# Kernel optimization log

Hardware: AMD Instinct MI355X
Metric: run time of the kernel (lower is better)

## Reference

```python
import jax, jax.numpy as jnp
import numpy as np

DIM_V = 512
NUM_HEADS = 8
LN_EPS = 1e-5


def _layernorm(x):
    # LayerNorm over last dim, no affine (simplified_layer_norm=True)
    mu = jnp.mean(x, axis=-1, keepdims=True)
    var = jnp.mean(jnp.square(x - mu), axis=-1, keepdims=True)
    return (x - mu) * jax.lax.rsqrt(var + LN_EPS)


def setup_inputs() -> dict:
    key = jax.random.key(0)
    ks = jax.random.split(key, 12)
    B, Nq, Nk, dQ, dK, dV = 16, 1024, 1024, 512, 512, DIM_V
    s = 0.02
    return {
        "Q": jax.random.normal(ks[0], (B, Nq, dQ), jnp.float32),
        "K": jax.random.normal(ks[1], (B, Nk, dK), jnp.float32),
        "Wq": jax.random.normal(ks[2], (dQ, dV), jnp.float32) * s,
        "bq": jnp.zeros((dV,), jnp.float32),
        "Wk": jax.random.normal(ks[3], (dK, dV), jnp.float32) * s,
        "bk": jnp.zeros((dV,), jnp.float32),
        "Wv": jax.random.normal(ks[4], (dK, dV), jnp.float32) * s,
        "bv": jnp.zeros((dV,), jnp.float32),
        "Wo": jax.random.normal(ks[5], (dV, dV), jnp.float32) * s,
        "bo": jnp.zeros((dV,), jnp.float32),
    }


def reference(Q, K, Wq, bq, Wk, bk, Wv, bv, Wo, bo):
    H = NUM_HEADS
    dh = DIM_V // H
    q = Q @ Wq + bq            # [B, Nq, dV]
    k = K @ Wk + bk            # [B, Nk, dV]
    v = K @ Wv + bv            # [B, Nk, dV]
    B, Nq, _ = q.shape
    Nk = k.shape[1]
    qh = q.reshape(B, Nq, H, dh)
    kh = k.reshape(B, Nk, H, dh)
    vh = v.reshape(B, Nk, H, dh)
    # NOTE: faithful to source — scale by sqrt(dim_V), not sqrt(head_dim)
    scores = jnp.einsum('bqhd,bkhd->bhqk', qh, kh) / jnp.sqrt(jnp.asarray(DIM_V, q.dtype))
    A = jax.nn.softmax(scores, axis=-1)                    # [B, H, Nq, Nk]
    attn = jnp.einsum('bhqk,bkhd->bqhd', A, vh).reshape(B, Nq, DIM_V)
    O = q + attn               # residual with projected Q
    O = _layernorm(O)          # ln0 (no affine)
    O = O + jax.nn.gelu(O @ Wo + bo, approximate=False)
    O = _layernorm(O)          # ln1 (no affine)
    return O
```

## Files before the change

kernel.cpp:

```cpp
#include <hip/hip_runtime.h>
#include <hip/hip_bf16.h>
#include <math.h>

typedef __bf16 bf16;
typedef __bf16 bf16x8 __attribute__((ext_vector_type(8)));
typedef float  f32x4  __attribute__((ext_vector_type(4)));

#define MFMA16(a,b,c) __builtin_amdgcn_mfma_f32_16x16x32_bf16((a),(b),(c),0,0,0)
#define ATT_SCALE_LOG2E 0.0637587160330163f

__device__ __forceinline__ void async16p(const void* g, void* l) {
    __builtin_amdgcn_global_load_lds((const __attribute__((address_space(1))) void*)g,
                                     (__attribute__((address_space(3))) void*)l,
                                     16, 0, 0);
}

__global__ __launch_bounds__(256) void prep_kernel(
    const float* __restrict__ Q, const float* __restrict__ K,
    const float* __restrict__ Wq, const float* __restrict__ Wk,
    const float* __restrict__ Wv, const float* __restrict__ Wo,
    bf16* __restrict__ Qb, bf16* __restrict__ Kb,
    bf16* __restrict__ WqT, bf16* __restrict__ WkT,
    bf16* __restrict__ WvT, bf16* __restrict__ WoT)
{
    __shared__ float tile[32][33];
    const int bx = blockIdx.x;
    if (bx < 8192) {
        const float* src = (bx < 4096) ? Q : K;
        bf16* dst        = (bx < 4096) ? Qb : Kb;
        int i = ((bx & 4095) * 256 + threadIdx.x) * 8;
        float4 a = *(const float4*)(src + i);
        float4 b = *(const float4*)(src + i + 4);
        bf16x8 o;
        o[0]=(bf16)a.x; o[1]=(bf16)a.y; o[2]=(bf16)a.z; o[3]=(bf16)a.w;
        o[4]=(bf16)b.x; o[5]=(bf16)b.y; o[6]=(bf16)b.z; o[7]=(bf16)b.w;
        *(bf16x8*)(dst + i) = o;
    } else {
        const int wid = bx - 8192;
        const float* W; bf16* T;
        switch (wid >> 8) {
          case 0: W=Wq; T=WqT; break;
          case 1: W=Wk; T=WkT; break;
          case 2: W=Wv; T=WvT; break;
          default: W=Wo; T=WoT; break;
        }
        const int rest = wid & 255;
        const int k0 = (rest & 15) * 32, n0 = (rest >> 4) * 32;
        const int tx = threadIdx.x & 31, ty = threadIdx.x >> 5;
        #pragma unroll
        for (int i=0;i<32;i+=8)
            tile[ty+i][tx] = W[(size_t)(k0+ty+i)*512 + n0+tx];
        __syncthreads();
        #pragma unroll
        for (int i=0;i<32;i+=8)
            T[(size_t)(n0+ty+i)*512 + k0+tx] = (bf16)tile[tx][ty+i];
    }
}

__device__ __forceinline__ void gemm_core(
    const bf16* __restrict__ A, const bf16* __restrict__ BT,
    int m0, int n0, char* smem, f32x4 (&acc)[4][4])
{
    bf16* As = (bf16*)smem;
    bf16* Bs = (bf16*)(smem + 16384);
    const int tid = threadIdx.x;
    const int lane = tid & 63, wave = tid >> 6;
    const int qd = lane >> 4, lr = lane & 15;
    const int wm = (wave & 1) * 64, wn = (wave >> 1) * 64;

    const int srow = tid >> 3;
    const int sgr  = ((tid & 7) ^ (srow & 7)) * 8;
    const bf16* gA = A  + (size_t)(m0 + srow)*512 + sgr;
    const bf16* gB = BT + (size_t)(n0 + srow)*512 + sgr;
    bf16* lA = As + wave*512;
    bf16* lB = Bs + wave*512;

    for (int k0 = 0; k0 < 512; k0 += 64) {
        __syncthreads();
        #pragma unroll
        for (int i=0;i<4;i++) {
            async16p(gA + k0 + (size_t)i*32*512, lA + i*2048);
            async16p(gB + k0 + (size_t)i*32*512, lB + i*2048);
        }
        __syncthreads();
        #pragma unroll
        for (int half=0; half<2; ++half) {
            bf16x8 af[4], bfr[4];
            #pragma unroll
            for (int mi=0;mi<4;mi++) {
                int row = wm + mi*16 + lr;
                af[mi] = *(bf16x8*)(As + row*64 + (((half*4+qd)^(lr&7))*8));
            }
            #pragma unroll
            for (int ni=0;ni<4;ni++) {
                int row = wn + ni*16 + lr;
                bfr[ni] = *(bf16x8*)(Bs + row*64 + (((half*4+qd)^(lr&7))*8));
            }
            #pragma unroll
            for (int mi=0;mi<4;mi++)
              #pragma unroll
              for (int ni=0;ni<4;ni++)
                acc[mi][ni] = MFMA16(af[mi], bfr[ni], acc[mi][ni]);
        }
    }
}

__global__ __launch_bounds__(256, 4) void gemm_qkv_kernel(
    const bf16* __restrict__ Qb, const bf16* __restrict__ Kb,
    const bf16* __restrict__ WqT, const bf16* __restrict__ WkT,
    const bf16* __restrict__ WvT,
    const float* __restrict__ bq, const float* __restrict__ bk,
    const float* __restrict__ bv,
    bf16* __restrict__ qbb, bf16* __restrict__ kbb, bf16* __restrict__ vT)
{
    __shared__ __align__(16) char smem[32768];
    const int z = blockIdx.z;
    const bf16* A  = (z == 0) ? Qb  : Kb;
    const bf16* BT = (z == 0) ? WqT : (z == 1) ? WkT : WvT;
    const float* bb = (z == 0) ? bq : (z == 1) ? bk  : bv;
    const int m0 = blockIdx.x * 128, n0 = blockIdx.y * 128;
    const int tid = threadIdx.x;
    const int lane = tid & 63, wave = tid >> 6;
    const int qd = lane >> 4, lr = lane & 15;
    const int wm = (wave & 1) * 64, wn = (wave >> 1) * 64;

    f32x4 acc[4][4];
    #pragma unroll
    for (int i=0;i<4;i++)
      #pragma unroll
      for (int j=0;j<4;j++) acc[i][j] = (f32x4){0,0,0,0};

    gemm_core(A, BT, m0, n0, smem, acc);

    if (z < 2) {
        bf16* C = (z == 0) ? qbb : kbb;
        #pragma unroll
        for (int ni=0;ni<4;ni++) {
            int n = n0 + wn + ni*16 + lr;
            float bv0 = bb[n];
            #pragma unroll
            for (int mi=0;mi<4;mi++) {
                int mb = m0 + wm + mi*16 + qd*4;
                #pragma unroll
                for (int r=0;r<4;r++)
                    C[(size_t)(mb+r)*512 + n] = (bf16)(acc[mi][ni][r] + bv0);
            }
        }
    } else {
        bf16* Lt = (bf16*)smem;
        const int b = m0 >> 10, tok0 = m0 & 1023;
        const int row = tid >> 2, ch = tid & 3;
        #pragma unroll
        for (int half = 0; half < 2; ++half) {
            __syncthreads();
            if ((wn >> 6) == half) {
                #pragma unroll
                for (int ni=0;ni<4;ni++) {
                    int nl = ni*16 + lr;
                    float bvv = bb[n0 + half*64 + nl];
                    #pragma unroll
                    for (int mi=0;mi<4;mi++)
                      #pragma unroll
                      for (int r=0;r<4;r++) {
                        int col = wm + mi*16 + qd*4 + r;
                        Lt[nl*128 + ((((col>>3)^(nl&7))<<3) | (col&7))]
                            = (bf16)(acc[mi][ni][r] + bvv);
                      }
                }
            }
            __syncthreads();
            const int h = (n0 >> 6) + half;
            bf16* dst = vT + ((size_t)((b*8 + h)*64 + row))*1024 + tok0 + ch*32;
            #pragma unroll
            for (int s=0;s<4;s++) {
                int g = (ch*4 + s) ^ (row & 7);
                *(uint4*)(dst + s*8) = *(uint4*)(Lt + row*128 + g*8);
            }
        }
    }
}

__global__ __launch_bounds__(256, 4) void attn_kernel(
    const bf16* __restrict__ qb, const bf16* __restrict__ kb,
    const bf16* __restrict__ vT, bf16* __restrict__ attnb)
{
    const int qt = blockIdx.x, h = blockIdx.y, b = blockIdx.z;
    const int tid = threadIdx.x, lane = tid & 63, wave = tid >> 6;
    const int qd = lane >> 4, lr = lane & 15;
    const int q0 = qt*128 + wave*32;

    __shared__ bf16 Ks[64*64];
    __shared__ bf16 Vs[64*64];
    __shared__ bf16 Pl[4][32][72];

    bf16x8 aq[2][2];
    #pragma unroll
    for (int mi=0;mi<2;mi++) {
        const bf16* qrow = qb + ((size_t)(b*1024 + q0 + mi*16 + lr))*512 + h*64;
        aq[mi][0] = *(const bf16x8*)(qrow + qd*8);
        aq[mi][1] = *(const bf16x8*)(qrow + 32 + qd*8);
    }

    const int srow = tid >> 2;
    const int c2 = (tid & 3) * 2;
    const int wg0 = ((c2  ) ^ (srow & 7)) * 8;
    const int wg1 = ((c2+1) ^ (srow & 7)) * 8;
    const bf16* kgp = kb + ((size_t)(b*1024 + srow))*512 + h*64 + c2*8;
    const bf16* vgp = vT + ((size_t)((b*8 + h)*64 + srow))*1024 + c2*8;

    uint4 k0r = *(const uint4*)(kgp);
    uint4 k1r = *(const uint4*)(kgp + 8);
    uint4 v0r = *(const uint4*)(vgp);
    uint4 v1r = *(const uint4*)(vgp + 8);

    f32x4 acc[2][4];
    #pragma unroll
    for (int mi=0;mi<2;mi++)
      #pragma unroll
      for (int ni=0;ni<4;ni++) acc[mi][ni] = (f32x4){0,0,0,0};
    float l[2][4] = {{0,0,0,0},{0,0,0,0}};

    for (int t=0; t<16; ++t) {
        __syncthreads();
        *(uint4*)(&Ks[srow*64 + wg0]) = k0r;
        *(uint4*)(&Ks[srow*64 + wg1]) = k1r;
        *(uint4*)(&Vs[srow*64 + wg0]) = v0r;
        *(uint4*)(&Vs[srow*64 + wg1]) = v1r;
        __syncthreads();
        if (t < 15) {
            const size_t kk = (size_t)(t+1)*64;
            k0r = *(const uint4*)(kgp + kk*512);
            k1r = *(const uint4*)(kgp + kk*512 + 8);
            v0r = *(const uint4*)(vgp + kk);
            v1r = *(const uint4*)(vgp + kk + 8);
        }

        f32x4 s[2][4];
        #pragma unroll
        for (int mi=0;mi<2;mi++)
          #pragma unroll
          for (int ni=0;ni<4;ni++) s[mi][ni] = (f32x4){0,0,0,0};
        #pragma unroll
        for (int ni=0;ni<4;ni++) {
            int row = ni*16 + lr;
            bf16x8 b0 = *(bf16x8*)(Ks + row*64 + (((qd  )^(lr&7))*8));
            bf16x8 b1 = *(bf16x8*)(Ks + row*64 + (((qd+4)^(lr&7))*8));
            #pragma unroll
            for (int mi=0;mi<2;mi++) {
                s[mi][ni] = MFMA16(aq[mi][0], b0, s[mi][ni]);
                s[mi][ni] = MFMA16(aq[mi][1], b1, s[mi][ni]);
            }
        }
        #pragma unroll
        for (int mi=0;mi<2;mi++)
          #pragma unroll
          for (int ni=0;ni<4;ni++)
            #pragma unroll
            for (int r=0;r<4;r++) {
                float pv = exp2f(s[mi][ni][r] * ATT_SCALE_LOG2E);
                s[mi][ni][r] = pv;
                l[mi][r] += pv;
            }
        #pragma unroll
        for (int mi=0;mi<2;mi++)
          #pragma unroll
          for (int ni=0;ni<4;ni++)
            #pragma unroll
            for (int r=0;r<4;r++)
                Pl[wave][mi*16 + qd*4 + r][ni*16 + lr] = (bf16)s[mi][ni][r];
        bf16x8 ap[2][2];
        #pragma unroll
        for (int mi=0;mi<2;mi++) {
            ap[mi][0] = *(bf16x8*)(&Pl[wave][mi*16+lr][qd*8]);
            ap[mi][1] = *(bf16x8*)(&Pl[wave][mi*16+lr][32+qd*8]);
        }
        #pragma unroll
        for (int ni=0;ni<4;ni++) {
            int row = ni*16 + lr;
            bf16x8 v0 = *(bf16x8*)(Vs + row*64 + (((qd  )^(lr&7))*8));
            bf16x8 v1 = *(bf16x8*)(Vs + row*64 + (((qd+4)^(lr&7))*8));
            #pragma unroll
            for (int mi=0;mi<2;mi++) {
                acc[mi][ni] = MFMA16(ap[mi][0], v0, acc[mi][ni]);
                acc[mi][ni] = MFMA16(ap[mi][1], v1, acc[mi][ni]);
            }
        }
    }

    #pragma unroll
    for (int off=1; off<16; off<<=1)
      #pragma unroll
      for (int mi=0;mi<2;mi++)
        #pragma unroll
        for (int r=0;r<4;r++) l[mi][r] += __shfl_xor(l[mi][r], off);

    #pragma unroll
    for (int mi=0;mi<2;mi++) {
        float inv[4];
        #pragma unroll
        for (int r=0;r<4;r++) inv[r] = 1.f / l[mi][r];
        #pragma unroll
        for (int ni=0;ni<4;ni++)
          #pragma unroll
          for (int r=0;r<4;r++)
            Pl[wave][qd*4+r][ni*16+lr] = (bf16)(acc[mi][ni][r] * inv[r]);
        bf16x8 oA = *(bf16x8*)(&Pl[wave][lr][qd*8]);
        bf16x8 oB = *(bf16x8*)(&Pl[wave][lr][32+qd*8]);
        bf16* dst = attnb + ((size_t)(b*1024 + q0 + mi*16 + lr))*512 + h*64;
        *(bf16x8*)(dst + qd*8)      = oA;
        *(bf16x8*)(dst + 32 + qd*8) = oB;
    }
}

__global__ __launch_bounds__(256) void ln0_kernel(
    const bf16* __restrict__ qbb, const bf16* __restrict__ attnb,
    bf16* __restrict__ Obf)
{
    const int wave = threadIdx.x >> 6, lane = threadIdx.x & 63;
    const int row = blockIdx.x*4 + wave;
    const size_t base = (size_t)row*512 + lane*8;
    bf16x8 qv = *(const bf16x8*)(qbb + base);
    bf16x8 av = *(const bf16x8*)(attnb + base);
    float x[8];
    #pragma unroll
    for (int i=0;i<8;i++) x[i] = (float)qv[i] + (float)av[i];
    float s1 = 0.f, s2 = 0.f;
    #pragma unroll
    for (int i=0;i<8;i++){ s1 += x[i]; s2 += x[i]*x[i]; }
    #pragma unroll
    for (int off=1; off<64; off<<=1) { s1 += __shfl_xor(s1, off); s2 += __shfl_xor(s2, off); }
    float mu  = s1 * (1.f/512.f);
    float var = s2 * (1.f/512.f) - mu*mu;
    float rstd = rsqrtf(var + 1e-5f);
    bf16x8 ob;
    #pragma unroll
    for (int i=0;i<8;i++) ob[i] = (bf16)((x[i]-mu)*rstd);
    *(bf16x8*)(Obf + base) = ob;
}

__global__ __launch_bounds__(256, 4) void gemm_o_kernel(
    const bf16* __restrict__ Obf, const bf16* __restrict__ WoT,
    const float* __restrict__ bo, bf16* __restrict__ xb)
{
    __shared__ __align__(16) char smem[32768];
    const int m0 = blockIdx.x * 128, n0 = blockIdx.y * 128;
    const int tid = threadIdx.x;
    const int lane = tid & 63, wave = tid >> 6;
    const int qd = lane >> 4, lr = lane & 15;
    const int wm = (wave & 1) * 64, wn = (wave >> 1) * 64;

    f32x4 acc[4][4];
    #pragma unroll
    for (int i=0;i<4;i++)
      #pragma unroll
      for (int j=0;j<4;j++) acc[i][j] = (f32x4){0,0,0,0};

    gemm_core(Obf, WoT, m0, n0, smem, acc);

    #pragma unroll
    for (int ni=0;ni<4;ni++) {
        int n = n0 + wn + ni*16 + lr;
        float bv = bo[n];
        #pragma unroll
        for (int mi=0;mi<4;mi++) {
            int mb = m0 + wm + mi*16 + qd*4;
            #pragma unroll
            for (int r=0;r<4;r++) {
                float g = acc[mi][ni][r] + bv;
                float gelu = 0.5f * g * (1.f + erff(g * 0.70710678118654752f));
                size_t idx = (size_t)(mb+r)*512 + n;
                xb[idx] = (bf16)((float)Obf[idx] + gelu);
            }
        }
    }
}

__global__ __launch_bounds__(256) void ln1_kernel(
    const bf16* __restrict__ xb, float* __restrict__ out)
{
    const int wave = threadIdx.x >> 6, lane = threadIdx.x & 63;
    const int row = blockIdx.x*4 + wave;
    const size_t base = (size_t)row*512 + lane*8;
    bf16x8 xv = *(const bf16x8*)(xb + base);
    float x[8];
    #pragma unroll
    for (int i=0;i<8;i++) x[i] = (float)xv[i];
    float s1 = 0.f, s2 = 0.f;
    #pragma unroll
    for (int i=0;i<8;i++){ s1 += x[i]; s2 += x[i]*x[i]; }
    #pragma unroll
    for (int off=1; off<64; off<<=1) { s1 += __shfl_xor(s1, off); s2 += __shfl_xor(s2, off); }
    float mu  = s1 * (1.f/512.f);
    float var = s2 * (1.f/512.f) - mu*mu;
    float rstd = rsqrtf(var + 1e-5f);
    float4 o0 = {(x[0]-mu)*rstd,(x[1]-mu)*rstd,(x[2]-mu)*rstd,(x[3]-mu)*rstd};
    float4 o1 = {(x[4]-mu)*rstd,(x[5]-mu)*rstd,(x[6]-mu)*rstd,(x[7]-mu)*rstd};
    *(float4*)(out + base)     = o0;
    *(float4*)(out + base + 4) = o1;
}

extern "C" void kernel_launch(void* const* d_in, const int* in_sizes, int n_in,
                              void* d_out, int out_size, void* d_ws, size_t ws_size,
                              hipStream_t stream)
{
    (void)in_sizes; (void)n_in; (void)out_size; (void)ws_size;
    const float* Q  = (const float*)d_in[0];
    const float* K  = (const float*)d_in[1];
    const float* Wq = (const float*)d_in[2];
    const float* bq = (const float*)d_in[3];
    const float* Wk = (const float*)d_in[4];
    const float* bk = (const float*)d_in[5];
    const float* Wv = (const float*)d_in[6];
    const float* bv = (const float*)d_in[7];
    const float* Wo = (const float*)d_in[8];
    const float* bo = (const float*)d_in[9];
    float* out = (float*)d_out;

    const size_t nTok = (size_t)16*1024*512;
    char* p = (char*)d_ws;
    auto alloc = [&](size_t bytes)->char* {
        char* r = p; p += (bytes + 255) & ~(size_t)255; return r;
    };
    bf16* Qb    = (bf16*)alloc(nTok*2);
    bf16* Kb    = (bf16*)alloc(nTok*2);
    bf16* WqT   = (bf16*)alloc(512*512*2);
    bf16* WkT   = (bf16*)alloc(512*512*2);
    bf16* WvT   = (bf16*)alloc(512*512*2);
    bf16* WoT   = (bf16*)alloc(512*512*2);
    bf16* qbb   = (bf16*)alloc(nTok*2);
    bf16* kbb   = (bf16*)alloc(nTok*2);
    bf16* vT    = (bf16*)alloc(nTok*2);
    bf16* attnb = (bf16*)alloc(nTok*2);
    bf16* Obf   = (bf16*)alloc(nTok*2);
    bf16* xb    = (bf16*)alloc(nTok*2);

    prep_kernel<<<9216, 256, 0, stream>>>(Q, K, Wq, Wk, Wv, Wo,
                                          Qb, Kb, WqT, WkT, WvT, WoT);
    gemm_qkv_kernel<<<dim3(128,4,3), 256, 0, stream>>>(Qb, Kb, WqT, WkT, WvT,
                                                       bq, bk, bv, qbb, kbb, vT);
    attn_kernel<<<dim3(8,8,16), 256, 0, stream>>>(qbb, kbb, vT, attnb);
    ln0_kernel<<<4096, 256, 0, stream>>>(qbb, attnb, Obf);
    gemm_o_kernel<<<dim3(128,4), 256, 0, stream>>>(Obf, WoT, bo, xb);
    ln1_kernel<<<4096, 256, 0, stream>>>(xb, out);
}
```

Before: 294.9 us.

## Fuse fp32-to-bf16 input conversion into QKV GEMM and residual into attention

Drops the separate pass that converts Q and K to bf16. The QKV GEMM now loads fp32 tiles straight into shared memory and converts them while building MFMA fragments, with the K-step halved to 32. The residual add of projected q is moved into the attention epilogue, so ln0 no longer reads qbb. The attention K/V shared tiles switch from an XOR swizzle to a padded layout, and exp2 with a folded log2e becomes __expf. This removes a full fp32 read/bf16 write round trip of the inputs, but the fp32 A tile doubles shared traffic per element and occupancy is lowered to 3.

```diff
diff --git a/kernel.cpp b/kernel.cpp
--- a/kernel.cpp
+++ b/kernel.cpp
@@ -7,7 +7,7 @@
 typedef float  f32x4  __attribute__((ext_vector_type(4)));
 
 #define MFMA16(a,b,c) __builtin_amdgcn_mfma_f32_16x16x32_bf16((a),(b),(c),0,0,0)
-#define ATT_SCALE_LOG2E 0.0637587160330163f
+#define ATT_SCALE 0.0441941738241592f
 
 __device__ __forceinline__ void async16p(const void* g, void* l) {
     __builtin_amdgcn_global_load_lds((const __attribute__((address_space(1))) void*)g,
@@ -15,122 +15,96 @@
                                      16, 0, 0);
 }
 
-__global__ __launch_bounds__(256) void prep_kernel(
-    const float* __restrict__ Q, const float* __restrict__ K,
+__global__ __launch_bounds__(256) void prep_w_kernel(
     const float* __restrict__ Wq, const float* __restrict__ Wk,
     const float* __restrict__ Wv, const float* __restrict__ Wo,
-    bf16* __restrict__ Qb, bf16* __restrict__ Kb,
     bf16* __restrict__ WqT, bf16* __restrict__ WkT,
     bf16* __restrict__ WvT, bf16* __restrict__ WoT)
 {
     __shared__ float tile[32][33];
     const int bx = blockIdx.x;
-    if (bx < 8192) {
-        const float* src = (bx < 4096) ? Q : K;
-        bf16* dst        = (bx < 4096) ? Qb : Kb;
-        int i = ((bx & 4095) * 256 + threadIdx.x) * 8;
-        float4 a = *(const float4*)(src + i);
-        float4 b = *(const float4*)(src + i + 4);
-        bf16x8 o;
-        o[0]=(bf16)a.x; o[1]=(bf16)a.y; o[2]=(bf16)a.z; o[3]=(bf16)a.w;
-        o[4]=(bf16)b.x; o[5]=(bf16)b.y; o[6]=(bf16)b.z; o[7]=(bf16)b.w;
-        *(bf16x8*)(dst + i) = o;
-    } else {
-        const int wid = bx - 8192;
-        const float* W; bf16* T;
-        switch (wid >> 8) {
-          case 0: W=Wq; T=WqT; break;
-          case 1: W=Wk; T=WkT; break;
-          case 2: W=Wv; T=WvT; break;
-          default: W=Wo; T=WoT; break;
-        }
-        const int rest = wid & 255;
-        const int k0 = (rest & 15) * 32, n0 = (rest >> 4) * 32;
-        const int tx = threadIdx.x & 31, ty = threadIdx.x >> 5;
-        #pragma unroll
-        for (int i=0;i<32;i+=8)
-            tile[ty+i][tx] = W[(size_t)(k0+ty+i)*512 + n0+tx];
-        __syncthreads();
-        #pragma unroll
-        for (int i=0;i<32;i+=8)
-            T[(size_t)(n0+ty+i)*512 + k0+tx] = (bf16)tile[tx][ty+i];
-    }
-}
-
-__device__ __forceinline__ void gemm_core(
-    const bf16* __restrict__ A, const bf16* __restrict__ BT,
-    int m0, int n0, char* smem, f32x4 (&acc)[4][4])
-{
-    bf16* As = (bf16*)smem;
-    bf16* Bs = (bf16*)(smem + 16384);
-    const int tid = threadIdx.x;
-    const int lane = tid & 63, wave = tid >> 6;
-    const int qd = lane >> 4, lr = lane & 15;
-    const int wm = (wave & 1) * 64, wn = (wave >> 1) * 64;
-
-    const int srow = tid >> 3;
-    const int sgr  = ((tid & 7) ^ (srow & 7)) * 8;
-    const bf16* gA = A  + (size_t)(m0 + srow)*512 + sgr;
-    const bf16* gB = BT + (size_t)(n0 + srow)*512 + sgr;
-    bf16* lA = As + wave*512;
-    bf16* lB = Bs + wave*512;
-
-    for (int k0 = 0; k0 < 512; k0 += 64) {
-        __syncthreads();
-        #pragma unroll
-        for (int i=0;i<4;i++) {
-            async16p(gA + k0 + (size_t)i*32*512, lA + i*2048);
-            async16p(gB + k0 + (size_t)i*32*512, lB + i*2048);
-        }
-        __syncthreads();
-        #pragma unroll
-        for (int half=0; half<2; ++half) {
-            bf16x8 af[4], bfr[4];
-            #pragma unroll
-            for (int mi=0;mi<4;mi++) {
-                int row = wm + mi*16 + lr;
-                af[mi] = *(bf16x8*)(As + row*64 + (((half*4+qd)^(lr&7))*8));
-            }
-            #pragma unroll
-            for (int ni=0;ni<4;ni++) {
-                int row = wn + ni*16 + lr;
-                bfr[ni] = *(bf16x8*)(Bs + row*64 + (((half*4+qd)^(lr&7))*8));
-            }
-            #pragma unroll
-            for (int mi=0;mi<4;mi++)
-              #pragma unroll
-              for (int ni=0;ni<4;ni++)
-                acc[mi][ni] = MFMA16(af[mi], bfr[ni], acc[mi][ni]);
-        }
-    }
-}
-
-__global__ __launch_bounds__(256, 4) void gemm_qkv_kernel(
-    const bf16* __restrict__ Qb, const bf16* __restrict__ Kb,
+    const float* W; bf16* T;
+    switch (bx >> 8) {
+      case 0: W=Wq; T=WqT; break;
+      case 1: W=Wk; T=WkT; break;
+      case 2: W=Wv; T=WvT; break;
+      default: W=Wo; T=WoT; break;
+    }
+    const int rest = bx & 255;
+    const int k0 = (rest & 15) * 32, n0 = (rest >> 4) * 32;
+    const int tx = threadIdx.x & 31, ty = threadIdx.x >> 5;
+    #pragma unroll
+    for (int i=0;i<32;i+=8)
+        tile[ty+i][tx] = W[(size_t)(k0+ty+i)*512 + n0+tx];
+    __syncthreads();
+    #pragma unroll
+    for (int i=0;i<32;i+=8)
+        T[(size_t)(n0+ty+i)*512 + k0+tx] = (bf16)tile[tx][ty+i];
+}
+
+__global__ __launch_bounds__(256, 3) void gemm_qkv_kernel(
+    const float* __restrict__ Qf, const float* __restrict__ Kf,
     const bf16* __restrict__ WqT, const bf16* __restrict__ WkT,
     const bf16* __restrict__ WvT,
     const float* __restrict__ bq, const float* __restrict__ bk,
     const float* __restrict__ bv,
     bf16* __restrict__ qbb, bf16* __restrict__ kbb, bf16* __restrict__ vT)
 {
-    __shared__ __align__(16) char smem[32768];
+    __shared__ __align__(16) char smem[24576];
+    float* As32 = (float*)smem;
+    bf16*  Bs   = (bf16*)(smem + 16384);
+    bf16*  Lt   = (bf16*)smem;
+
     const int z = blockIdx.z;
-    const bf16* A  = (z == 0) ? Qb  : Kb;
-    const bf16* BT = (z == 0) ? WqT : (z == 1) ? WkT : WvT;
-    const float* bb = (z == 0) ? bq : (z == 1) ? bk  : bv;
+    const float* A  = (z == 0) ? Qf  : Kf;
+    const bf16*  BT = (z == 0) ? WqT : (z == 1) ? WkT : WvT;
+    const float* bb = (z == 0) ? bq  : (z == 1) ? bk  : bv;
+
     const int m0 = blockIdx.x * 128, n0 = blockIdx.y * 128;
     const int tid = threadIdx.x;
     const int lane = tid & 63, wave = tid >> 6;
     const int qd = lane >> 4, lr = lane & 15;
     const int wm = (wave & 1) * 64, wn = (wave >> 1) * 64;
 
+    const float* gA = A + (size_t)(m0 + (tid>>3))*512 + (((tid&7)^((tid>>3)&7))*4);
+    float* lA = As32 + wave*256;
+    const bf16* gB = BT + (size_t)(n0 + (tid>>2))*512 + (((tid&3)^((tid>>2)&3))*8);
+    bf16* lB = Bs + wave*512;
+
     f32x4 acc[4][4];
     #pragma unroll
     for (int i=0;i<4;i++)
       #pragma unroll
       for (int j=0;j<4;j++) acc[i][j] = (f32x4){0,0,0,0};
 
-    gemm_core(A, BT, m0, n0, smem, acc);
+    for (int k0 = 0; k0 < 512; k0 += 32) {
+        __syncthreads();
+        #pragma unroll
+        for (int i=0;i<4;i++)
+            async16p(gA + k0 + (size_t)i*32*512, lA + i*1024);
+        async16p(gB + k0,          lB);
+        async16p(gB + k0 + 64*512, lB + 2048);
+        __syncthreads();
+        bf16x8 af[4], bfr[4];
+        #pragma unroll
+        for (int mi=0;mi<4;mi++) {
+            int row = wm + mi*16 + lr;
+            f32x4 f0 = *(f32x4*)(As32 + row*32 + (((qd*2  )^(lr&7))*4));
+            f32x4 f1 = *(f32x4*)(As32 + row*32 + (((qd*2+1)^(lr&7))*4));
+            bf16x8 a;
+            a[0]=(bf16)f0[0]; a[1]=(bf16)f0[1]; a[2]=(bf16)f0[2]; a[3]=(bf16)f0[3];
+            a[4]=(bf16)f1[0]; a[5]=(bf16)f1[1]; a[6]=(bf16)f1[2]; a[7]=(bf16)f1[3];
+            af[mi] = a;
+        }
+        #pragma unroll
+        for (int ni=0;ni<4;ni++)
+            bfr[ni] = *(bf16x8*)(Bs + (wn+ni*16+lr)*32 + ((qd^(lr&3))*8));
+        #pragma unroll
+        for (int mi=0;mi<4;mi++)
+          #pragma unroll
+          for (int ni=0;ni<4;ni++)
+            acc[mi][ni] = MFMA16(af[mi], bfr[ni], acc[mi][ni]);
+    }
 
     if (z < 2) {
         bf16* C = (z == 0) ? qbb : kbb;
@@ -147,7 +121,6 @@
             }
         }
     } else {
-        bf16* Lt = (bf16*)smem;
         const int b = m0 >> 10, tok0 = m0 & 1023;
         const int row = tid >> 2, ch = tid & 3;
         #pragma unroll
@@ -189,8 +162,8 @@
     const int qd = lane >> 4, lr = lane & 15;
     const int q0 = qt*128 + wave*32;
 
-    __shared__ bf16 Ks[64*64];
-    __shared__ bf16 Vs[64*64];
+    __shared__ bf16 Ks[64][72];
+    __shared__ bf16 Vs[64][72];
     __shared__ bf16 Pl[4][32][72];
 
     bf16x8 aq[2][2];
@@ -202,11 +175,9 @@
     }
 
     const int srow = tid >> 2;
-    const int c2 = (tid & 3) * 2;
-    const int wg0 = ((c2  ) ^ (srow & 7)) * 8;
-    const int wg1 = ((c2+1) ^ (srow & 7)) * 8;
-    const bf16* kgp = kb + ((size_t)(b*1024 + srow))*512 + h*64 + c2*8;
-    const bf16* vgp = vT + ((size_t)((b*8 + h)*64 + srow))*1024 + c2*8;
+    const int scol = (tid & 3) * 16;
+    const bf16* kgp = kb + ((size_t)(b*1024 + srow))*512 + h*64 + scol;
+    const bf16* vgp = vT + ((size_t)((b*8 + h)*64 + srow))*1024 + scol;
 
     uint4 k0r = *(const uint4*)(kgp);
     uint4 k1r = *(const uint4*)(kgp + 8);
@@ -222,10 +193,10 @@
 
     for (int t=0; t<16; ++t) {
         __syncthreads();
-        *(uint4*)(&Ks[srow*64 + wg0]) = k0r;
-        *(uint4*)(&Ks[srow*64 + wg1]) = k1r;
-        *(uint4*)(&Vs[srow*64 + wg0]) = v0r;
-        *(uint4*)(&Vs[srow*64 + wg1]) = v1r;
+        *(uint4*)(&Ks[srow][scol])   = k0r;
+        *(uint4*)(&Ks[srow][scol+8]) = k1r;
+        *(uint4*)(&Vs[srow][scol])   = v0r;
+        *(uint4*)(&Vs[srow][scol+8]) = v1r;
         __syncthreads();
         if (t < 15) {
             const size_t kk = (size_t)(t+1)*64;
@@ -242,9 +213,8 @@
           for (int ni=0;ni<4;ni++) s[mi][ni] = (f32x4){0,0,0,0};
         #pragma unroll
         for (int ni=0;ni<4;ni++) {
-            int row = ni*16 + lr;
-            bf16x8 b0 = *(bf16x8*)(Ks + row*64 + (((qd  )^(lr&7))*8));
-            bf16x8 b1 = *(bf16x8*)(Ks + row*64 + (((qd+4)^(lr&7))*8));
+            bf16x8 b0 = *(bf16x8*)(&Ks[ni*16+lr][qd*8]);
+            bf16x8 b1 = *(bf16x8*)(&Ks[ni*16+lr][32+qd*8]);
             #pragma unroll
             for (int mi=0;mi<2;mi++) {
                 s[mi][ni] = MFMA16(aq[mi][0], b0, s[mi][ni]);
@@ -257,7 +227,7 @@
           for (int ni=0;ni<4;ni++)
             #pragma unroll
             for (int r=0;r<4;r++) {
-                float pv = exp2f(s[mi][ni][r] * ATT_SCALE_LOG2E);
+                float pv = __expf(s[mi][ni][r] * ATT_SCALE);
                 s[mi][ni][r] = pv;
                 l[mi][r] += pv;
             }
@@ -276,9 +246,8 @@
         }
         #pragma unroll
         for (int ni=0;ni<4;ni++) {
-            int row = ni*16 + lr;
-            bf16x8 v0 = *(bf16x8*)(Vs + row*64 + (((qd  )^(lr&7))*8));
-            bf16x8 v1 = *(bf16x8*)(Vs + row*64 + (((qd+4)^(lr&7))*8));
+            bf16x8 v0 = *(bf16x8*)(&Vs[ni*16+lr][qd*8]);
+            bf16x8 v1 = *(bf16x8*)(&Vs[ni*16+lr][32+qd*8]);
             #pragma unroll
             for (int mi=0;mi<2;mi++) {
                 acc[mi][ni] = MFMA16(ap[mi][0], v0, acc[mi][ni]);
@@ -306,24 +275,28 @@
             Pl[wave][qd*4+r][ni*16+lr] = (bf16)(acc[mi][ni][r] * inv[r]);
         bf16x8 oA = *(bf16x8*)(&Pl[wave][lr][qd*8]);
         bf16x8 oB = *(bf16x8*)(&Pl[wave][lr][32+qd*8]);
+        bf16x8 rA, rB;
+        #pragma unroll
+        for (int j=0;j<8;j++) {
+            rA[j] = (bf16)((float)oA[j] + (float)aq[mi][0][j]);
+            rB[j] = (bf16)((float)oB[j] + (float)aq[mi][1][j]);
+        }
         bf16* dst = attnb + ((size_t)(b*1024 + q0 + mi*16 + lr))*512 + h*64;
-        *(bf16x8*)(dst + qd*8)      = oA;
-        *(bf16x8*)(dst + 32 + qd*8) = oB;
+        *(bf16x8*)(dst + qd*8)      = rA;
+        *(bf16x8*)(dst + 32 + qd*8) = rB;
     }
 }
 
 __global__ __launch_bounds__(256) void ln0_kernel(
-    const bf16* __restrict__ qbb, const bf16* __restrict__ attnb,
-    bf16* __restrict__ Obf)
+    const bf16* __restrict__ attnb, bf16* __restrict__ Obf)
 {
     const int wave = threadIdx.x >> 6, lane = threadIdx.x & 63;
     const int row = blockIdx.x*4 + wave;
     const size_t base = (size_t)row*512 + lane*8;
-    bf16x8 qv = *(const bf16x8*)(qbb + base);
     bf16x8 av = *(const bf16x8*)(attnb + base);
     float x[8];
     #pragma unroll
-    for (int i=0;i<8;i++) x[i] = (float)qv[i] + (float)av[i];
+    for (int i=0;i<8;i++) x[i] = (float)av[i];
     float s1 = 0.f, s2 = 0.f;
     #pragma unroll
     for (int i=0;i<8;i++){ s1 += x[i]; s2 += x[i]*x[i]; }
@@ -336,6 +309,54 @@
     #pragma unroll
     for (int i=0;i<8;i++) ob[i] = (bf16)((x[i]-mu)*rstd);
     *(bf16x8*)(Obf + base) = ob;
+}
+
+__device__ __forceinline__ void gemm_core(
+    const bf16* __restrict__ A, const bf16* __restrict__ BT,
+    int m0, int n0, char* smem, f32x4 (&acc)[4][4])
+{
+    bf16* As = (bf16*)smem;
+    bf16* Bs = (bf16*)(smem + 16384);
+    const int tid = threadIdx.x;
+    const int lane = tid & 63, wave = tid >> 6;
+    const int qd = lane >> 4, lr = lane & 15;
+    const int wm = (wave & 1) * 64, wn = (wave >> 1) * 64;
+
+    const int srow = tid >> 3;
+    const int sgr  = ((tid & 7) ^ (srow & 7)) * 8;
+    const bf16* gA = A  + (size_t)(m0 + srow)*512 + sgr;
+    const bf16* gB = BT + (size_t)(n0 + srow)*512 + sgr;
+    bf16* lA = As + wave*512;
+    bf16* lB = Bs + wave*512;
+
+    for (int k0 = 0; k0 < 512; k0 += 64) {
+        __syncthreads();
+        #pragma unroll
+        for (int i=0;i<4;i++) {
+            async16p(gA + k0 + (size_t)i*32*512, lA + i*2048);
+            async16p(gB + k0 + (size_t)i*32*512, lB + i*2048);
+        }
+        __syncthreads();
+        #pragma unroll
+        for (int half=0; half<2; ++half) {
+            bf16x8 af[4], bfr[4];
+            #pragma unroll
+            for (int mi=0;mi<4;mi++) {
+                int row = wm + mi*16 + lr;
+                af[mi] = *(bf16x8*)(As + row*64 + (((half*4+qd)^(lr&7))*8));
+            }
+            #pragma unroll
+            for (int ni=0;ni<4;ni++) {
+                int row = wn + ni*16 + lr;
+                bfr[ni] = *(bf16x8*)(Bs + row*64 + (((half*4+qd)^(lr&7))*8));
+            }
+            #pragma unroll
+            for (int mi=0;mi<4;mi++)
+              #pragma unroll
+              for (int ni=0;ni<4;ni++)
+                acc[mi][ni] = MFMA16(af[mi], bfr[ni], acc[mi][ni]);
+        }
+    }
 }
 
 __global__ __launch_bounds__(256, 4) void gemm_o_kernel(
@@ -421,8 +442,6 @@
     auto alloc = [&](size_t bytes)->char* {
         char* r = p; p += (bytes + 255) & ~(size_t)255; return r;
     };
-    bf16* Qb    = (bf16*)alloc(nTok*2);
-    bf16* Kb    = (bf16*)alloc(nTok*2);
     bf16* WqT   = (bf16*)alloc(512*512*2);
     bf16* WkT   = (bf16*)alloc(512*512*2);
     bf16* WvT   = (bf16*)alloc(512*512*2);
@@ -434,12 +453,11 @@
     bf16* Obf   = (bf16*)alloc(nTok*2);
     bf16* xb    = (bf16*)alloc(nTok*2);
 
-    prep_kernel<<<9216, 256, 0, stream>>>(Q, K, Wq, Wk, Wv, Wo,
-                                          Qb, Kb, WqT, WkT, WvT, WoT);
-    gemm_qkv_kernel<<<dim3(128,4,3), 256, 0, stream>>>(Qb, Kb, WqT, WkT, WvT,
+    prep_w_kernel<<<1024, 256, 0, stream>>>(Wq, Wk, Wv, Wo, WqT, WkT, WvT, WoT);
+    gemm_qkv_kernel<<<dim3(128,4,3), 256, 0, stream>>>(Q, K, WqT, WkT, WvT,
                                                        bq, bk, bv, qbb, kbb, vT);
     attn_kernel<<<dim3(8,8,16), 256, 0, stream>>>(qbb, kbb, vT, attnb);
-    ln0_kernel<<<4096, 256, 0, stream>>>(qbb, attnb, Obf);
+    ln0_kernel<<<4096, 256, 0, stream>>>(attnb, Obf);
     gemm_o_kernel<<<dim3(128,4), 256, 0, stream>>>(Obf, WoT, bo, xb);
     ln1_kernel<<<4096, 256, 0, stream>>>(xb, out);
 }
```

Measured after the change: 270.6 us. -8.2%, faster.
